# Optimization experiments

Hardware: AMD Instinct MI355X
Metric: run time of the kernel (lower is better)

The kernel has to match this reference:

```python
import jax, jax.numpy as jnp
import numpy as np

N = 50000      # nodes
E = 800000     # directed edges (avg degree 16)
F_IN = 128     # dataset.num_features
H = 256        # hidden_channels
C = 40         # dataset.num_classes


def _glorot(k, shape):
    lim = float(np.sqrt(6.0 / (shape[0] + shape[1])))
    return jax.random.uniform(k, shape, jnp.float32, -lim, lim)


def setup_inputs() -> dict:
    key = jax.random.key(0)
    ks = jax.random.split(key, 8)
    x = jax.random.normal(ks[0], (N, F_IN), jnp.float32)
    edge_index = jax.random.randint(ks[1], (2, E), 0, N, dtype=jnp.int32)
    W1 = _glorot(ks[2], (F_IN, H));      b1 = jnp.zeros((H,), jnp.float32)
    W2 = _glorot(ks[3], (H, H // 2));    b2 = jnp.zeros((H // 2,), jnp.float32)
    W3 = _glorot(ks[4], (H // 2, H // 4)); b3 = jnp.zeros((H // 4,), jnp.float32)
    W4 = _glorot(ks[5], (H // 4, C));    b4 = jnp.zeros((C,), jnp.float32)
    return {"x": x, "edge_index": edge_index,
            "W1": W1, "b1": b1, "W2": W2, "b2": b2,
            "W3": W3, "b3": b3, "W4": W4, "b4": b4}


def reference(x, edge_index, W1, b1, W2, b2, W3, b3, W4, b4):
    # GCNConv with default add_self_loops=True and symmetric normalization.
    loops = jnp.arange(N, dtype=edge_index.dtype)
    src = jnp.concatenate([edge_index[0], loops])   # message sources
    dst = jnp.concatenate([edge_index[1], loops])   # aggregation targets
    # degree computed on target index (PyG default), incl. self-loops
    deg = jax.ops.segment_sum(jnp.ones_like(dst, jnp.float32), dst, num_segments=N)
    dinv = jnp.where(deg > 0, jax.lax.rsqrt(deg), 0.0)
    norm = dinv[src] * dinv[dst]                    # [E+N]

    def conv(h, W, b):
        h = h @ W                                   # transform first (PyG order)
        msg = h[src] * norm[:, None]                # gather + scale
        return jax.ops.segment_sum(msg, dst, num_segments=N) + b

    h = jax.nn.relu(conv(x, W1, b1))   # dropout = identity in eval mode
    h = jax.nn.relu(conv(h, W2, b2))
    h = jax.nn.relu(conv(h, W3, b3))
    return conv(h, W4, b4)
```

## Files before the change

kernel.cpp:

```cpp
#include <hip/hip_runtime.h>
#include <stdint.h>

#define NNODES 50000
#define NEDGES 800000
#define NB ((NNODES + 255) / 256)
#define EPB 4096
#define SCAT_NBLK ((NEDGES + EPB - 1) / EPB)
#define AGG_BLOCKS 2048

typedef __attribute__((ext_vector_type(8))) short bf16x8;
typedef __attribute__((ext_vector_type(4))) float f32x4;

__device__ inline unsigned short f2bf(float f) {
    unsigned u = __float_as_uint(f);
    return (unsigned short)((u + 0x7fffu + ((u >> 16) & 1u)) >> 16);
}
__device__ inline float bf2f(unsigned short h) {
    return __uint_as_float(((unsigned)h) << 16);
}


__global__ void zero_kernel(int* __restrict__ p, int n) {
    int i = blockIdx.x * blockDim.x + threadIdx.x;
    if (i < n) p[i] = 0;
}

__global__ __launch_bounds__(256) void bucket_count_kernel(const int* __restrict__ dst,
                                                           int* __restrict__ bhist) {
    __shared__ int h[NB];
    for (int b = threadIdx.x; b < NB; b += 256) h[b] = 0;
    __syncthreads();
    const int base = blockIdx.x * EPB;
#pragma unroll
    for (int i = 0; i < EPB / 256; ++i) {
        const int e = base + threadIdx.x + i * 256;
        if (e < NEDGES) atomicAdd(&h[dst[e] >> 8], 1);
    }
    __syncthreads();
    for (int b = threadIdx.x; b < NB; b += 256)
        if (h[b]) atomicAdd(&bhist[b], h[b]);
}

__global__ __launch_bounds__(256) void bucket_scan_kernel(const int* __restrict__ bhist,
                                                          int* __restrict__ bofs,
                                                          int* __restrict__ gcur,
                                                          int* __restrict__ rp_last) {
    __shared__ int s[256];
    const int t = threadIdx.x;
    s[t] = (t < NB) ? bhist[t] : 0;
    __syncthreads();
    for (int off = 1; off < 256; off <<= 1) {
        int v = (t >= off) ? s[t - off] : 0;
        __syncthreads();
        s[t] += v;
        __syncthreads();
    }
    if (t < NB) {
        const int excl = (t > 0) ? s[t - 1] : 0;
        bofs[t] = excl;
        gcur[t] = excl;
    }
    if (t == 255) { bofs[NB] = s[255]; rp_last[0] = s[255]; }
}

__global__ __launch_bounds__(256) void bucket_scatter_kernel(const int* __restrict__ src,
                                                             const int* __restrict__ dst,
                                                             int* __restrict__ gcur,
                                                             unsigned* __restrict__ gpk) {
    __shared__ int h[256];
    __shared__ int s[256];
    __shared__ int gof[256];
    __shared__ unsigned pr[EPB];
    __shared__ int ga[EPB];

    const int t = threadIdx.x;
    const int base = blockIdx.x * EPB;
    const int nval = min(EPB, NEDGES - base);

    h[t] = 0;
    __syncthreads();
#pragma unroll
    for (int i = 0; i < EPB / 256; ++i) {
        const int e = base + t + i * 256;
        if (e < NEDGES) atomicAdd(&h[dst[e] >> 8], 1);
    }
    __syncthreads();
    s[t] = h[t];
    __syncthreads();
    for (int off = 1; off < 256; off <<= 1) {
        int v = (t >= off) ? s[t - off] : 0;
        __syncthreads();
        s[t] += v;
        __syncthreads();
    }
    {
        const int c = h[t];
        if (t < NB && c > 0) gof[t] = atomicAdd(&gcur[t], c);
        const int lofs = s[t] - c;
        h[t] = lofs;
        s[t] = lofs;
    }
    __syncthreads();
#pragma unroll
    for (int i = 0; i < EPB / 256; ++i) {
        const int e = base + t + i * 256;
        if (e < NEDGES) {
            const int d = dst[e];
            const int b = d >> 8;
            const int slot = atomicAdd(&h[b], 1);
            pr[slot] = ((unsigned)(d & 255) << 16) | (unsigned)src[e];
            ga[slot] = gof[b] + (slot - s[b]);
        }
    }
    __syncthreads();
#pragma unroll
    for (int i = 0; i < EPB / 256; ++i) {
        const int slot = t + i * 256;
        if (slot < nval) gpk[ga[slot]] = pr[slot];
    }
}

__global__ __launch_bounds__(256) void csr_fill_kernel(const unsigned* __restrict__ gpk,
                                                       const int* __restrict__ bofs,
                                                       int* __restrict__ rp,
                                                       float* __restrict__ dinv,
                                                       unsigned short* __restrict__ col) {
    __shared__ int c[256];
    __shared__ int s[256];
    __shared__ int cur[256];
    const int t = threadIdx.x;
    const int b = blockIdx.x;
    const int beg = bofs[b], end = bofs[b + 1];
    c[t] = 0;
    __syncthreads();
    for (int e = beg + t; e < end; e += 256) atomicAdd(&c[gpk[e] >> 16], 1);
    __syncthreads();
    s[t] = c[t];
    __syncthreads();
    for (int off = 1; off < 256; off <<= 1) {
        int v = (t >= off) ? s[t - off] : 0;
        __syncthreads();
        s[t] += v;
        __syncthreads();
    }
    const int excl = s[t] - c[t];
    cur[t] = excl;
    const int node = b * 256 + t;
    if (node < NNODES) {
        rp[node] = beg + excl;
        dinv[node] = rsqrtf((float)(c[t] + 1));
    }
    __syncthreads();
    for (int e = beg + t; e < end; e += 256) {
        const unsigned p = gpk[e];
        const int r = atomicAdd(&cur[p >> 16], 1);
        col[beg + r] = (unsigned short)(p & 0xffffu);
    }
}


__global__ __launch_bounds__(256) void cvt_kernel(const float* __restrict__ in,
                                                  const float* __restrict__ dinv,
                                                  unsigned short* __restrict__ out, int n4) {
    int i = blockIdx.x * 256 + threadIdx.x;
    if (i >= n4) return;
    const float dv = dinv[i >> 5];
    float4 v = *(const float4*)(in + (size_t)i * 4);
    ushort4 h;
    h.x = f2bf(dv * v.x); h.y = f2bf(dv * v.y); h.z = f2bf(dv * v.z); h.w = f2bf(dv * v.w);
    *(ushort4*)(out + (size_t)i * 4) = h;
}


template <bool RELU, bool HAS_BIAS>
__global__ __launch_bounds__(256) void agg128_kernel(const float* __restrict__ in32,
                                                     const unsigned short* __restrict__ inbf,
                                                     float* __restrict__ out,
                                                     const int* __restrict__ rp,
                                                     const unsigned short* __restrict__ col,
                                                     const float* __restrict__ dinv,
                                                     const float* __restrict__ bias) {
    const int wave = threadIdx.x >> 6;
    const int lane = threadIdx.x & 63;
    const int quarter = lane >> 4;
    const int fl = lane & 15;
    const int dstride = gridDim.x * 4;

    for (int d = blockIdx.x * 4 + wave; d < NNODES; d += dstride) {
        const float dv = dinv[d];

        float acc[8] = {0.f, 0.f, 0.f, 0.f, 0.f, 0.f, 0.f, 0.f};
        if (quarter == 0) {
            float4 s0 = *(const float4*)(in32 + (size_t)d * 128 + fl * 8);
            float4 s1 = *(const float4*)(in32 + (size_t)d * 128 + fl * 8 + 4);
            acc[0] = dv * s0.x; acc[1] = dv * s0.y; acc[2] = dv * s0.z; acc[3] = dv * s0.w;
            acc[4] = dv * s1.x; acc[5] = dv * s1.y; acc[6] = dv * s1.z; acc[7] = dv * s1.w;
        }

        int j = rp[d] + quarter;
        const int end = rp[d + 1];
        for (; j + 12 < end; j += 16) {
            const int c0 = col[j], c1 = col[j + 4], c2 = col[j + 8], c3 = col[j + 12];
            bf16x8 a0 = *(const bf16x8*)(inbf + (size_t)c0 * 128 + fl * 8);
            bf16x8 a1 = *(const bf16x8*)(inbf + (size_t)c1 * 128 + fl * 8);
            bf16x8 a2 = *(const bf16x8*)(inbf + (size_t)c2 * 128 + fl * 8);
            bf16x8 a3 = *(const bf16x8*)(inbf + (size_t)c3 * 128 + fl * 8);
#pragma unroll
            for (int k = 0; k < 8; ++k)
                acc[k] += (bf2f((unsigned short)a0[k]) + bf2f((unsigned short)a1[k])) +
                          (bf2f((unsigned short)a2[k]) + bf2f((unsigned short)a3[k]));
        }
        for (; j + 4 < end; j += 8) {
            const int c0 = col[j], c1 = col[j + 4];
            bf16x8 a0 = *(const bf16x8*)(inbf + (size_t)c0 * 128 + fl * 8);
            bf16x8 a1 = *(const bf16x8*)(inbf + (size_t)c1 * 128 + fl * 8);
#pragma unroll
            for (int k = 0; k < 8; ++k)
                acc[k] += bf2f((unsigned short)a0[k]) + bf2f((unsigned short)a1[k]);
        }
        if (j < end) {
            const int c0 = col[j];
            bf16x8 a0 = *(const bf16x8*)(inbf + (size_t)c0 * 128 + fl * 8);
#pragma unroll
            for (int k = 0; k < 8; ++k) acc[k] += bf2f((unsigned short)a0[k]);
        }

#pragma unroll
        for (int v = 0; v < 8; ++v) {
            acc[v] += __shfl_down(acc[v], 32);
            acc[v] += __shfl_down(acc[v], 16);
        }

        if (quarter == 0) {
            float r[8];
#pragma unroll
            for (int v = 0; v < 8; ++v) {
                float t = dv * acc[v];
                if constexpr (HAS_BIAS) t += bias[fl * 8 + v];
                if constexpr (RELU) t = fmaxf(t, 0.0f);
                r[v] = t;
            }
            *(float4*)(out + (size_t)d * 128 + fl * 8)     = make_float4(r[0], r[1], r[2], r[3]);
            *(float4*)(out + (size_t)d * 128 + fl * 8 + 4) = make_float4(r[4], r[5], r[6], r[7]);
        }
    }
}

template <bool RELU, bool HAS_BIAS, bool WRITE_BF>
__global__ __launch_bounds__(256) void agg64_kernel(const float* __restrict__ in32,
                                                    const unsigned short* __restrict__ inbf,
                                                    float* __restrict__ out,
                                                    unsigned short* __restrict__ outbf,
                                                    const int* __restrict__ rp,
                                                    const unsigned short* __restrict__ col,
                                                    const float* __restrict__ dinv,
                                                    const float* __restrict__ bias) {
    const int wave = threadIdx.x >> 6;
    const int lane = threadIdx.x & 63;
    const int eighth = lane >> 3;
    const int fl = lane & 7;
    const int dstride = gridDim.x * 4;

    for (int d = blockIdx.x * 4 + wave; d < NNODES; d += dstride) {
        const float dv = dinv[d];

        float acc[8] = {0.f, 0.f, 0.f, 0.f, 0.f, 0.f, 0.f, 0.f};
        if (eighth == 0) {
            float4 s0 = *(const float4*)(in32 + (size_t)d * 64 + fl * 8);
            float4 s1 = *(const float4*)(in32 + (size_t)d * 64 + fl * 8 + 4);
            acc[0] = dv * s0.x; acc[1] = dv * s0.y; acc[2] = dv * s0.z; acc[3] = dv * s0.w;
            acc[4] = dv * s1.x; acc[5] = dv * s1.y; acc[6] = dv * s1.z; acc[7] = dv * s1.w;
        }

        int j = rp[d] + eighth;
        const int end = rp[d + 1];
        for (; j + 8 < end; j += 16) {
            const int c0 = col[j], c1 = col[j + 8];
            bf16x8 a0 = *(const bf16x8*)(inbf + (size_t)c0 * 64 + fl * 8);
            bf16x8 a1 = *(const bf16x8*)(inbf + (size_t)c1 * 64 + fl * 8);
#pragma unroll
            for (int k = 0; k < 8; ++k)
                acc[k] += bf2f((unsigned short)a0[k]) + bf2f((unsigned short)a1[k]);
        }
        if (j < end) {
            const int c0 = col[j];
            bf16x8 a0 = *(const bf16x8*)(inbf + (size_t)c0 * 64 + fl * 8);
#pragma unroll
            for (int k = 0; k < 8; ++k) acc[k] += bf2f((unsigned short)a0[k]);
        }

#pragma unroll
        for (int v = 0; v < 8; ++v) {
            acc[v] += __shfl_down(acc[v], 32);
            acc[v] += __shfl_down(acc[v], 16);
            acc[v] += __shfl_down(acc[v], 8);
        }

        if (eighth == 0) {
            float r[8];
#pragma unroll
            for (int v = 0; v < 8; ++v) {
                float t = dv * acc[v];
                if constexpr (HAS_BIAS) t += bias[fl * 8 + v];
                if constexpr (RELU) t = fmaxf(t, 0.0f);
                r[v] = t;
            }
            *(float4*)(out + (size_t)d * 64 + fl * 8)     = make_float4(r[0], r[1], r[2], r[3]);
            *(float4*)(out + (size_t)d * 64 + fl * 8 + 4) = make_float4(r[4], r[5], r[6], r[7]);
            if constexpr (WRITE_BF) {
                ushort4 h0, h1;
                h0.x = f2bf(dv * r[0]); h0.y = f2bf(dv * r[1]);
                h0.z = f2bf(dv * r[2]); h0.w = f2bf(dv * r[3]);
                h1.x = f2bf(dv * r[4]); h1.y = f2bf(dv * r[5]);
                h1.z = f2bf(dv * r[6]); h1.w = f2bf(dv * r[7]);
                *(ushort4*)(outbf + (size_t)d * 64 + fl * 8)     = h0;
                *(ushort4*)(outbf + (size_t)d * 64 + fl * 8 + 4) = h1;
            }
        }
    }
}


template <int K, int M>
__global__ __launch_bounds__(256) void repack_kernel(const float* __restrict__ W,
                                                     unsigned short* __restrict__ hi,
                                                     unsigned short* __restrict__ lo) {
    int i = blockIdx.x * 256 + threadIdx.x;
    if (i >= K * M) return;
    const int k = i / M, n = i % M;
    constexpr int KS = K / 32;
    const int cb = n >> 7;
    const int ct = (n >> 4) & 7;
    const int ln = ((k >> 3) & 3) * 16 + (n & 15);
    const int j  = k & 7;
    const int ks = k >> 5;
    const size_t o = ((((size_t)cb * KS + ks) * 8 + ct) * 64 + ln) * 8 + j;
    const float f = W[i];
    const unsigned short h = f2bf(f);
    hi[o] = h;
    lo[o] = f2bf(f - bf2f(h));
}


template <int K, int M, int BM, bool BIAS_RELU, bool WRITE_BF>
__global__ __launch_bounds__(256) void mfma_gemm_kernel(const float* __restrict__ A,
                                                        const unsigned short* __restrict__ Whi,
                                                        const unsigned short* __restrict__ Wlo,
                                                        const float* __restrict__ bias,
                                                        float* __restrict__ C,
                                                        unsigned short* __restrict__ Cbf,
                                                        const float* __restrict__ dinv) {
    constexpr int KS = K / 32;
    constexpr int ASZ = BM * 64;
    constexpr int CI = (BM == 128) ? 4 : 2;
    __shared__ char lds[2 * ASZ + 16384];
    char* Ahi = lds;
    char* Alo = lds + ASZ;
    char* Bhi = lds + 2 * ASZ;
    char* Blo = lds + 2 * ASZ + 8192;

    const int t = threadIdx.x;
    const int lane = t & 63;
    const int w = t >> 6;
    const int wr = (BM == 128) ? (w >> 1) : 0;
    const int wc = (BM == 128) ? (w & 1) : w;
    const int r0 = blockIdx.x * BM;
    const int n0 = blockIdx.y * 128;

    const unsigned short* bhg = Whi + (size_t)blockIdx.y * KS * 4096;
    const unsigned short* blg = Wlo + (size_t)blockIdx.y * KS * 4096;

    f32x4 acc[4][CI];
#pragma unroll
    for (int i = 0; i < 4; ++i)
#pragma unroll
        for (int j = 0; j < CI; ++j) acc[i][j] = (f32x4){0.f, 0.f, 0.f, 0.f};

    for (int ks = 0; ks < KS; ++ks) {
        const int k0 = ks * 32;

        {
            const char* gh = (const char*)(bhg + (size_t)ks * 4096);
            const char* gl = (const char*)(blg + (size_t)ks * 4096);
#pragma unroll
            for (int c = 0; c < 2; ++c) {
                const int ct = w * 2 + c;
                __builtin_amdgcn_global_load_lds(
                    (const __attribute__((address_space(1))) void*)(gh + ct * 1024 + lane * 16),
                    (__attribute__((address_space(3))) void*)(Bhi + ct * 1024), 16, 0, 0);
                __builtin_amdgcn_global_load_lds(
                    (const __attribute__((address_space(1))) void*)(gl + ct * 1024 + lane * 16),
                    (__attribute__((address_space(3))) void*)(Blo + ct * 1024), 16, 0, 0);
            }
        }

        float4 av[BM / 32];
#pragma unroll
        for (int i = 0; i < BM / 32; ++i) {
            const int q = t + i * 256;
            const int row = q >> 3;
            const int kq = (q & 7) * 4;
            const int gr = r0 + row;
            float4 v = make_float4(0.f, 0.f, 0.f, 0.f);
            if (gr < NNODES) v = *(const float4*)(A + (size_t)gr * K + k0 + kq);
            av[i] = v;
        }
#pragma unroll
        for (int i = 0; i < BM / 32; ++i) {
            const int q = t + i * 256;
            const int row = q >> 3;
            const int kq = (q & 7) * 4;
            const int rt = row >> 4, m = row & 15, quad = kq >> 3, j0 = kq & 7;
            const int off = rt * 1024 + (quad * 16 + m) * 16 + j0 * 2;
            const float4 v = av[i];
            ushort4 h, l;
            h.x = f2bf(v.x); l.x = f2bf(v.x - bf2f(h.x));
            h.y = f2bf(v.y); l.y = f2bf(v.y - bf2f(h.y));
            h.z = f2bf(v.z); l.z = f2bf(v.z - bf2f(h.z));
            h.w = f2bf(v.w); l.w = f2bf(v.w - bf2f(h.w));
            *(ushort4*)(Ahi + off) = h;
            *(ushort4*)(Alo + off) = l;
        }
        __syncthreads();

        bf16x8 ah[4], al[4], bh[CI], bl[CI];
#pragma unroll
        for (int i = 0; i < 4; ++i) {
            ah[i] = *(const bf16x8*)(Ahi + (wr * 4 + i) * 1024 + lane * 16);
            al[i] = *(const bf16x8*)(Alo + (wr * 4 + i) * 1024 + lane * 16);
        }
#pragma unroll
        for (int j = 0; j < CI; ++j) {
            bh[j] = *(const bf16x8*)(Bhi + (wc * CI + j) * 1024 + lane * 16);
            bl[j] = *(const bf16x8*)(Blo + (wc * CI + j) * 1024 + lane * 16);
        }
#pragma unroll
        for (int i = 0; i < 4; ++i)
#pragma unroll
            for (int j = 0; j < CI; ++j) {
                acc[i][j] = __builtin_amdgcn_mfma_f32_16x16x32_bf16(ah[i], bh[j], acc[i][j], 0, 0, 0);
                acc[i][j] = __builtin_amdgcn_mfma_f32_16x16x32_bf16(ah[i], bl[j], acc[i][j], 0, 0, 0);
                acc[i][j] = __builtin_amdgcn_mfma_f32_16x16x32_bf16(al[i], bh[j], acc[i][j], 0, 0, 0);
            }
        __syncthreads();
    }

    const int quad = lane >> 4;
    const int cl = lane & 15;
#pragma unroll
    for (int i = 0; i < 4; ++i) {
#pragma unroll
        for (int j = 0; j < CI; ++j) {
            const int colg = n0 + wc * (CI * 16) + j * 16 + cl;
            float bv = 0.f;
            if constexpr (BIAS_RELU) bv = bias[colg];
#pragma unroll
            for (int r = 0; r < 4; ++r) {
                const int rowg = r0 + wr * 64 + i * 16 + quad * 4 + r;
                if (rowg < NNODES) {
                    float v = acc[i][j][r] + bv;
                    if constexpr (BIAS_RELU) v = fmaxf(v, 0.f);
                    C[(size_t)rowg * M + colg] = v;
                    if constexpr (WRITE_BF) Cbf[(size_t)rowg * M + colg] = f2bf(dinv[rowg] * v);
                }
            }
        }
    }
}


template <int BM, int BN, int BK, int TM, int TN, bool HAS_BIAS, bool RELU, bool WRITE_BF>
__global__ __launch_bounds__(256) void gemm_kernel(const float* __restrict__ A,
                                                   const float* __restrict__ W,
                                                   const float* __restrict__ bias,
                                                   float* __restrict__ C,
                                                   unsigned short* __restrict__ Cbf,
                                                   const float* __restrict__ dinv,
                                                   int Nrows, int K, int M) {
    constexpr int TX = BN / TN;
    constexpr int TY = BM / TM;
    static_assert(TX * TY == 256, "thread grid must be 256");
    constexpr int A_LOADS = (BM * BK) / (256 * 4);
    constexpr int W_LOADS = (BN * BK) / (256 * 4);
    static_assert(A_LOADS >= 1 && W_LOADS >= 1, "tile too small");

    const int tid = threadIdx.x;
    const int tx = tid % TX;
    const int ty = tid / TX;
    const int r0 = blockIdx.x * BM;
    const int c0 = blockIdx.y * BN;

    __shared__ float As[BK][BM + 4];
    __shared__ float Ws[BK][BN];

    float acc[TM][TN] = {};

    for (int k0 = 0; k0 < K; k0 += BK) {
#pragma unroll
        for (int l = 0; l < A_LOADS; ++l) {
            const int idx = tid + l * 256;
            const int row = idx / (BK / 4);
            const int kq = idx % (BK / 4);
            float4 v = make_float4(0.f, 0.f, 0.f, 0.f);
            const int gr = r0 + row;
            if (gr < Nrows) v = *(const float4*)(A + (size_t)gr * K + k0 + kq * 4);
            As[kq * 4 + 0][row] = v.x;
            As[kq * 4 + 1][row] = v.y;
            As[kq * 4 + 2][row] = v.z;
            As[kq * 4 + 3][row] = v.w;
        }
#pragma unroll
        for (int l = 0; l < W_LOADS; ++l) {
            const int idx = tid + l * 256;
            const int kk = idx / (BN / 4);
            const int cq = idx % (BN / 4);
            const int gc = c0 + cq * 4;
            float4 v;
            const float* wrow = W + (size_t)(k0 + kk) * M;
            if (gc + 3 < M) {
                v = *(const float4*)(wrow + gc);
            } else {
                v.x = (gc + 0 < M) ? wrow[gc + 0] : 0.f;
                v.y = (gc + 1 < M) ? wrow[gc + 1] : 0.f;
                v.z = (gc + 2 < M) ? wrow[gc + 2] : 0.f;
                v.w = (gc + 3 < M) ? wrow[gc + 3] : 0.f;
            }
            *(float4*)&Ws[kk][cq * 4] = v;
        }
        __syncthreads();

#pragma unroll
        for (int kk = 0; kk < BK; ++kk) {
            float a[TM], b[TN];
#pragma unroll
            for (int i = 0; i < TM; ++i) a[i] = As[kk][ty * TM + i];
#pragma unroll
            for (int j = 0; j < TN; ++j) b[j] = Ws[kk][tx * TN + j];
#pragma unroll
            for (int i = 0; i < TM; ++i)
#pragma unroll
                for (int j = 0; j < TN; ++j) acc[i][j] += a[i] * b[j];
        }
        __syncthreads();
    }

#pragma unroll
    for (int i = 0; i < TM; ++i) {
        const int gr = r0 + ty * TM + i;
        if (gr >= Nrows) continue;
        const float dvr = WRITE_BF ? dinv[gr] : 0.f;
#pragma unroll
        for (int j = 0; j < TN; ++j) {
            const int gc = c0 + tx * TN + j;
            if (gc >= M) continue;
            float v = acc[i][j];
            if constexpr (HAS_BIAS) v += bias[gc];
            if constexpr (RELU) v = fmaxf(v, 0.0f);
            C[(size_t)gr * M + gc] = v;
            if constexpr (WRITE_BF) Cbf[(size_t)gr * M + gc] = f2bf(dvr * v);
        }
    }
}


extern "C" void kernel_launch(void* const* d_in, const int* in_sizes, int n_in,
                              void* d_out, int out_size, void* d_ws, size_t ws_size,
                              hipStream_t stream) {
    const float* x  = (const float*)d_in[0];
    const int* ei   = (const int*)d_in[1];
    const float* W1 = (const float*)d_in[2];
    const float* b1 = (const float*)d_in[3];
    const float* W2 = (const float*)d_in[4];
    const float* b2 = (const float*)d_in[5];
    const float* W3 = (const float*)d_in[6];
    const float* b3 = (const float*)d_in[7];
    const float* W4 = (const float*)d_in[8];
    const float* b4 = (const float*)d_in[9];
    float* out = (float*)d_out;
    const int* esrc = ei;
    const int* edst = ei + NEDGES;

    char* w = (char*)d_ws;
    auto alloc = [&](size_t bytes) -> void* {
        void* p = (void*)w;
        w += (bytes + 255) & ~(size_t)255;
        return p;
    };
    int* rp     = (int*)alloc((size_t)(NNODES + 1) * 4);
    unsigned short* col = (unsigned short*)alloc((size_t)NEDGES * 2);
    float* dinv = (float*)alloc((size_t)NNODES * 4);
    int* bhist  = (int*)alloc((size_t)NB * 4);
    int* bofs   = (int*)alloc((size_t)(NB + 1) * 4);
    int* gcur   = (int*)alloc((size_t)NB * 4);
    unsigned* gpk = (unsigned*)alloc((size_t)NEDGES * 4);
    unsigned short* W1hi = (unsigned short*)alloc((size_t)128 * 256 * 2);
    unsigned short* W1lo = (unsigned short*)alloc((size_t)128 * 256 * 2);
    unsigned short* W2hi = (unsigned short*)alloc((size_t)256 * 128 * 2);
    unsigned short* W2lo = (unsigned short*)alloc((size_t)256 * 128 * 2);
    float* B0   = (float*)alloc((size_t)NNODES * 256 * 4);
    float* B1   = (float*)alloc((size_t)NNODES * 128 * 4);
    float* B2   = (float*)alloc((size_t)NNODES * 128 * 4);
    unsigned short* xbf  = (unsigned short*)alloc((size_t)NNODES * 128 * 2);
    unsigned short* B1bf = (unsigned short*)alloc((size_t)NNODES * 128 * 2);
    unsigned short* B0bf = (unsigned short*)alloc((size_t)NNODES * 64 * 2);
    unsigned short* B3bf = (unsigned short*)alloc((size_t)NNODES * 64 * 2);

    repack_kernel<128, 256><<<(128 * 256 + 255) / 256, 256, 0, stream>>>(W1, W1hi, W1lo);
    repack_kernel<256, 128><<<(256 * 128 + 255) / 256, 256, 0, stream>>>(W2, W2hi, W2lo);

    zero_kernel<<<1, 256, 0, stream>>>(bhist, NB);
    bucket_count_kernel<<<SCAT_NBLK, 256, 0, stream>>>(edst, bhist);
    bucket_scan_kernel<<<1, 256, 0, stream>>>(bhist, bofs, gcur, rp + NNODES);
    bucket_scatter_kernel<<<SCAT_NBLK, 256, 0, stream>>>(esrc, edst, gcur, gpk);
    csr_fill_kernel<<<NB, 256, 0, stream>>>(gpk, bofs, rp, dinv, col);

    cvt_kernel<<<(NNODES * 128 / 4 + 255) / 256, 256, 0, stream>>>(x, dinv, xbf, NNODES * 128 / 4);

    const int rowBlks64 = (NNODES + 63) / 64;

    agg128_kernel<false, false><<<AGG_BLOCKS, 256, 0, stream>>>(x, xbf, B2, rp, col, dinv, nullptr);
    mfma_gemm_kernel<128, 256, 64, true, false>
        <<<dim3(rowBlks64, 2), 256, 0, stream>>>(B2, W1hi, W1lo, b1, B0, nullptr, nullptr);

    mfma_gemm_kernel<256, 128, 64, false, true>
        <<<dim3(rowBlks64, 1), 256, 0, stream>>>(B0, W2hi, W2lo, nullptr, B1, B1bf, dinv);
    agg128_kernel<true, true><<<AGG_BLOCKS, 256, 0, stream>>>(B1, B1bf, B2, rp, col, dinv, b2);

    gemm_kernel<64, 64, 16, 4, 4, false, false, true>
        <<<dim3(rowBlks64, 1), 256, 0, stream>>>(B2, W3, nullptr, B0, B0bf, dinv, NNODES, 128, 64);
    agg64_kernel<true, true, true><<<AGG_BLOCKS, 256, 0, stream>>>(B0, B0bf, B1, B3bf, rp, col, dinv, b3);

    agg64_kernel<false, false, false><<<AGG_BLOCKS, 256, 0, stream>>>(B1, B3bf, B2, nullptr, rp, col, dinv, nullptr);
    gemm_kernel<64, 64, 16, 4, 4, true, false, false>
        <<<dim3(rowBlks64, 1), 256, 0, stream>>>(B2, W4, b4, out, nullptr, nullptr, NNODES, 64, 40);
}
```

Baseline: 328.1 us.

## Scatter edges into fixed-capacity buckets, dropping count and scan passes

Replaces the count/scan/scatter CSR build with a direct scatter into fixed-size per-bucket regions, taking bucket offsets from atomic counters. Each CSR fill block scans the counters itself. Counter zeroing is folded into the weight repack kernel. This removes three kernel launches and one pass over the edge destinations, but uses a larger scratch buffer and assumes no bucket exceeds its fixed capacity.

```diff
diff --git a/kernel.cpp b/kernel.cpp
--- a/kernel.cpp
+++ b/kernel.cpp
@@ -6,6 +6,7 @@
 #define NB ((NNODES + 255) / 256)
 #define EPB 4096
 #define SCAT_NBLK ((NEDGES + EPB - 1) / EPB)
+#define BUCKCAP 8192
 #define AGG_BLOCKS 2048
 
 typedef __attribute__((ext_vector_type(8))) short bf16x8;
@@ -20,50 +21,7 @@
 }
 
 
-__global__ void zero_kernel(int* __restrict__ p, int n) {
-    int i = blockIdx.x * blockDim.x + threadIdx.x;
-    if (i < n) p[i] = 0;
-}
-
-__global__ __launch_bounds__(256) void bucket_count_kernel(const int* __restrict__ dst,
-                                                           int* __restrict__ bhist) {
-    __shared__ int h[NB];
-    for (int b = threadIdx.x; b < NB; b += 256) h[b] = 0;
-    __syncthreads();
-    const int base = blockIdx.x * EPB;
-#pragma unroll
-    for (int i = 0; i < EPB / 256; ++i) {
-        const int e = base + threadIdx.x + i * 256;
-        if (e < NEDGES) atomicAdd(&h[dst[e] >> 8], 1);
-    }
-    __syncthreads();
-    for (int b = threadIdx.x; b < NB; b += 256)
-        if (h[b]) atomicAdd(&bhist[b], h[b]);
-}
-
-__global__ __launch_bounds__(256) void bucket_scan_kernel(const int* __restrict__ bhist,
-                                                          int* __restrict__ bofs,
-                                                          int* __restrict__ gcur,
-                                                          int* __restrict__ rp_last) {
-    __shared__ int s[256];
-    const int t = threadIdx.x;
-    s[t] = (t < NB) ? bhist[t] : 0;
-    __syncthreads();
-    for (int off = 1; off < 256; off <<= 1) {
-        int v = (t >= off) ? s[t - off] : 0;
-        __syncthreads();
-        s[t] += v;
-        __syncthreads();
-    }
-    if (t < NB) {
-        const int excl = (t > 0) ? s[t - 1] : 0;
-        bofs[t] = excl;
-        gcur[t] = excl;
-    }
-    if (t == 255) { bofs[NB] = s[255]; rp_last[0] = s[255]; }
-}
-
-__global__ __launch_bounds__(256) void bucket_scatter_kernel(const int* __restrict__ src,
+__global__ __launch_bounds__(256) void scatter_direct_kernel(const int* __restrict__ src,
                                                              const int* __restrict__ dst,
                                                              int* __restrict__ gcur,
                                                              unsigned* __restrict__ gpk) {
@@ -109,7 +67,7 @@
             const int b = d >> 8;
             const int slot = atomicAdd(&h[b], 1);
             pr[slot] = ((unsigned)(d & 255) << 16) | (unsigned)src[e];
-            ga[slot] = gof[b] + (slot - s[b]);
+            ga[slot] = b * BUCKCAP + gof[b] + (slot - s[b]);
         }
     }
     __syncthreads();
@@ -120,20 +78,34 @@
     }
 }
 
-__global__ __launch_bounds__(256) void csr_fill_kernel(const unsigned* __restrict__ gpk,
-                                                       const int* __restrict__ bofs,
-                                                       int* __restrict__ rp,
-                                                       float* __restrict__ dinv,
-                                                       unsigned short* __restrict__ col) {
+__global__ __launch_bounds__(256) void csr_fill2_kernel(const unsigned* __restrict__ gpk,
+                                                        const int* __restrict__ gcur,
+                                                        int* __restrict__ rp,
+                                                        float* __restrict__ dinv,
+                                                        unsigned short* __restrict__ col) {
     __shared__ int c[256];
     __shared__ int s[256];
     __shared__ int cur[256];
     const int t = threadIdx.x;
     const int b = blockIdx.x;
-    const int beg = bofs[b], end = bofs[b + 1];
+
+    s[t] = (t < NB) ? gcur[t] : 0;
+    __syncthreads();
+    for (int off = 1; off < 256; off <<= 1) {
+        int v = (t >= off) ? s[t - off] : 0;
+        __syncthreads();
+        s[t] += v;
+        __syncthreads();
+    }
+    const int beg = (b > 0) ? s[b - 1] : 0;
+    const int cnt = s[b] - beg;
+    if (b == 0 && t == 255) rp[NNODES] = s[255];
+    __syncthreads();
+
+    const unsigned* g = gpk + (size_t)b * BUCKCAP;
     c[t] = 0;
     __syncthreads();
-    for (int e = beg + t; e < end; e += 256) atomicAdd(&c[gpk[e] >> 16], 1);
+    for (int e = t; e < cnt; e += 256) atomicAdd(&c[g[e] >> 16], 1);
     __syncthreads();
     s[t] = c[t];
     __syncthreads();
@@ -151,8 +123,8 @@
         dinv[node] = rsqrtf((float)(c[t] + 1));
     }
     __syncthreads();
-    for (int e = beg + t; e < end; e += 256) {
-        const unsigned p = gpk[e];
+    for (int e = t; e < cnt; e += 256) {
+        const unsigned p = g[e];
         const int r = atomicAdd(&cur[p >> 16], 1);
         col[beg + r] = (unsigned short)(p & 0xffffu);
     }
@@ -324,8 +296,10 @@
 template <int K, int M>
 __global__ __launch_bounds__(256) void repack_kernel(const float* __restrict__ W,
                                                      unsigned short* __restrict__ hi,
-                                                     unsigned short* __restrict__ lo) {
+                                                     unsigned short* __restrict__ lo,
+                                                     int* __restrict__ zbuf, int zn) {
     int i = blockIdx.x * 256 + threadIdx.x;
+    if (i < zn) zbuf[i] = 0;
     if (i >= K * M) return;
     const int k = i / M, n = i % M;
     constexpr int KS = K / 32;
@@ -589,10 +563,8 @@
     int* rp     = (int*)alloc((size_t)(NNODES + 1) * 4);
     unsigned short* col = (unsigned short*)alloc((size_t)NEDGES * 2);
     float* dinv = (float*)alloc((size_t)NNODES * 4);
-    int* bhist  = (int*)alloc((size_t)NB * 4);
-    int* bofs   = (int*)alloc((size_t)(NB + 1) * 4);
     int* gcur   = (int*)alloc((size_t)NB * 4);
-    unsigned* gpk = (unsigned*)alloc((size_t)NEDGES * 4);
+    unsigned* gpk = (unsigned*)alloc((size_t)NB * BUCKCAP * 4);
     unsigned short* W1hi = (unsigned short*)alloc((size_t)128 * 256 * 2);
     unsigned short* W1lo = (unsigned short*)alloc((size_t)128 * 256 * 2);
     unsigned short* W2hi = (unsigned short*)alloc((size_t)256 * 128 * 2);
@@ -605,14 +577,11 @@
     unsigned short* B0bf = (unsigned short*)alloc((size_t)NNODES * 64 * 2);
     unsigned short* B3bf = (unsigned short*)alloc((size_t)NNODES * 64 * 2);
 
-    repack_kernel<128, 256><<<(128 * 256 + 255) / 256, 256, 0, stream>>>(W1, W1hi, W1lo);
-    repack_kernel<256, 128><<<(256 * 128 + 255) / 256, 256, 0, stream>>>(W2, W2hi, W2lo);
-
-    zero_kernel<<<1, 256, 0, stream>>>(bhist, NB);
-    bucket_count_kernel<<<SCAT_NBLK, 256, 0, stream>>>(edst, bhist);
-    bucket_scan_kernel<<<1, 256, 0, stream>>>(bhist, bofs, gcur, rp + NNODES);
-    bucket_scatter_kernel<<<SCAT_NBLK, 256, 0, stream>>>(esrc, edst, gcur, gpk);
-    csr_fill_kernel<<<NB, 256, 0, stream>>>(gpk, bofs, rp, dinv, col);
+    repack_kernel<128, 256><<<(128 * 256 + 255) / 256, 256, 0, stream>>>(W1, W1hi, W1lo, gcur, NB);
+    repack_kernel<256, 128><<<(256 * 128 + 255) / 256, 256, 0, stream>>>(W2, W2hi, W2lo, nullptr, 0);
+
+    scatter_direct_kernel<<<SCAT_NBLK, 256, 0, stream>>>(esrc, edst, gcur, gpk);
+    csr_fill2_kernel<<<NB, 256, 0, stream>>>(gpk, gcur, rp, dinv, col);
 
     cvt_kernel<<<(NNODES * 128 / 4 + 255) / 256, 256, 0, stream>>>(x, dinv, xbf, NNODES * 128 / 4);
 
```

New measurement: 320.2 us (median of 2 runs). 2.4% less time.
